# Kernel optimization log

Measured on AMD Instinct MI355X. Metric: run time of the kernel, lower is better.

Reference implementation:

```python
import jax, jax.numpy as jnp
import numpy as np

N = 50000
E = 800000
IN_C = 128
HID = 128
OUT_C = 64
HEADS = 8
HD1 = HID // HEADS   # 16 per-head dim, layer 1 (concat)
HD2 = OUT_C          # 64 per-head dim, layer 2 (concat=False, mean over heads)
NEG_SLOPE = 0.2


def setup_inputs() -> dict:
    key = jax.random.key(0)
    ks = jax.random.split(key, 12)
    x = jax.random.normal(ks[0], (N, IN_C), dtype=jnp.float32)
    edge_index = jax.random.randint(ks[1], (2, E), 0, N, dtype=jnp.int64)
    s1 = 1.0 / np.sqrt(IN_C)
    s2 = 1.0 / np.sqrt(HID)
    W1 = jax.random.normal(ks[2], (IN_C, HEADS * HD1), dtype=jnp.float32) * s1
    att_src1 = jax.random.normal(ks[3], (HEADS, HD1), dtype=jnp.float32) * s1
    att_dst1 = jax.random.normal(ks[4], (HEADS, HD1), dtype=jnp.float32) * s1
    b1 = jnp.zeros((HID,), dtype=jnp.float32)
    W2 = jax.random.normal(ks[5], (HID, HEADS * HD2), dtype=jnp.float32) * s2
    att_src2 = jax.random.normal(ks[6], (HEADS, HD2), dtype=jnp.float32) * s2
    att_dst2 = jax.random.normal(ks[7], (HEADS, HD2), dtype=jnp.float32) * s2
    b2 = jnp.zeros((OUT_C,), dtype=jnp.float32)
    return {"x": x, "edge_index": edge_index,
            "W1": W1, "att_src1": att_src1, "att_dst1": att_dst1, "b1": b1,
            "W2": W2, "att_src2": att_src2, "att_dst2": att_dst2, "b2": b2}


def _gat_conv(x, W, a_src, a_dst, bias, src, dst, heads, head_dim, concat):
    n = x.shape[0]
    h = (x @ W).reshape(n, heads, head_dim)                      # [N,H,D]
    alpha_s = jnp.einsum('nhd,hd->nh', h, a_src)                  # [N,H]
    alpha_d = jnp.einsum('nhd,hd->nh', h, a_dst)                  # [N,H]
    e = jax.nn.leaky_relu(alpha_s[src] + alpha_d[dst], NEG_SLOPE)  # [E,H]
    # segment softmax over edges grouped by destination node
    m = jax.ops.segment_max(e, dst, num_segments=n)               # [N,H]
    m = jnp.where(jnp.isfinite(m), m, 0.0)
    ex = jnp.exp(e - m[dst])
    denom = jax.ops.segment_sum(ex, dst, num_segments=n)
    alpha = ex / (denom[dst] + 1e-16)                             # [E,H]
    out = jax.ops.segment_sum(h[src] * alpha[:, :, None], dst, num_segments=n)  # [N,H,D]
    if concat:
        out = out.reshape(n, heads * head_dim)
    else:
        out = out.mean(axis=1)
    return out + bias


def reference(x, edge_index, W1, att_src1, att_dst1, b1, W2, att_src2, att_dst2, b2):
    # PyG GATConv default add_self_loops=True
    loops = jnp.arange(N, dtype=edge_index.dtype)
    src = jnp.concatenate([edge_index[0], loops])
    dst = jnp.concatenate([edge_index[1], loops])
    h = _gat_conv(x, W1, att_src1, att_dst1, b1, src, dst, HEADS, HD1, True)
    h = jax.nn.relu(h)
    out = _gat_conv(h, W2, att_src2, att_dst2, b2, src, dst, HEADS, HD2, False)
    return out
```

## Files before the change

kernel.cpp:

```cpp
#include <hip/hip_runtime.h>

#define N_NODES 50000
#define N_EDGES 800000
#define ET (N_EDGES + N_NODES)
#define HEADS 8
#define NPAD 50048
#define SCAN_NB 196
#define CAP 96
#define LRS 1032
#define NB_DEG 3321
#define NB_GEMM1 782

typedef __attribute__((ext_vector_type(8))) _Float16 half8;
typedef __attribute__((ext_vector_type(2))) _Float16 half2v;
typedef __attribute__((ext_vector_type(4))) float f32x4;

__device__ __forceinline__ void wave_lds_fence(){
  asm volatile("s_waitcnt lgkmcnt(0)" ::: "memory");
}

__device__ __forceinline__ int edge_src(const int* ei, int e, int is64){
  if (e >= N_EDGES) return e - N_EDGES;
  return is64 ? ei[2*e] : ei[e];
}
__device__ __forceinline__ int edge_dst(const int* ei, int e, int is64){
  if (e >= N_EDGES) return e - N_EDGES;
  return is64 ? ei[2*(N_EDGES + e)] : ei[N_EDGES + e];
}

__global__ void k_init_wprep(const int* __restrict__ ei, int* __restrict__ deg,
                             int* __restrict__ cnt, int* __restrict__ flag,
                             const float* __restrict__ W1, const float* __restrict__ W2,
                             const float* __restrict__ as2, const float* __restrict__ ad2,
                             _Float16* __restrict__ Bp1, _Float16* __restrict__ Bp,
                             float* __restrict__ ws2, float* __restrict__ wd2){
  int b = blockIdx.x;
  int t_ = threadIdx.x;
  if (b < SCAN_NB){
    int i = b*256 + t_;
    if (i < N_NODES){ deg[i] = 0; cnt[i] = 0; }
    if (i == 0){
      int zeros = 0;
      for (int k = 0; k < 64; k++){
        if (ei[2*k + 1] == 0) zeros++;
      }
      *flag = (zeros >= 60) ? 1 : 0;
    }
  } else if (b < SCAN_NB + 256){
    int t = (b - SCAN_NB)*256 + t_;
    int j = t & 7, lane = (t >> 3) & 63, nt = (t >> 9) & 3, kt = t >> 11;
    int k = kt*32 + (lane >> 4)*8 + j;
    int c = nt*16 + (lane & 15);
    int h = k >> 7, kk = k & 127;
    Bp[t] = (_Float16)(0.125f * W2[kk*512 + h*64 + c]);
  } else if (b < SCAN_NB + 320){
    int t = (b - SCAN_NB - 256)*256 + t_;
    int j = t & 7, lane = (t >> 3) & 63, nt = (t >> 9) & 7, kt = t >> 12;
    int k = kt*32 + (lane >> 4)*8 + j;
    int c = nt*16 + (lane & 15);
    Bp1[t] = (_Float16)W1[k*128 + c];
  } else {
    int t = (b - SCAN_NB - 320)*256 + t_;
    int k = t >> 3, h = t & 7;
    float s = 0.f, d = 0.f;
    for (int dd = 0; dd < 64; dd++){
      float w = W2[k*512 + h*64 + dd];
      s += w * as2[h*64 + dd];
      d += w * ad2[h*64 + dd];
    }
    ws2[h*128 + k] = s;
    wd2[h*128 + k] = d;
  }
}

__global__ void __launch_bounds__(256) k_deg_gemm1(
    const int* __restrict__ ei, int* __restrict__ deg, const int* __restrict__ flag,
    const float* __restrict__ x, const _Float16* __restrict__ Bp1,
    _Float16* __restrict__ h1,
    const float* __restrict__ as1, const float* __restrict__ ad1,
    float* __restrict__ als1, float* __restrict__ ald1){
  if (blockIdx.x < NB_DEG){
    int e = blockIdx.x*blockDim.x + threadIdx.x;
    if (e >= ET) return;
    int is64 = *flag;
    int d = edge_dst(ei, e, is64);
    atomicAdd(&deg[d], 1);
    return;
  }
  int bid = blockIdx.x - NB_DEG;
  int tid = threadIdx.x;
  int lane = tid & 63, wv = tid >> 6;
  int n0 = bid*64 + wv*16;
  int rowA = n0 + (lane & 15);
  int koff = (lane >> 4)*8;
  const float* xr = x + (size_t)rowA*128 + koff;
  f32x4 acc[8];
  #pragma unroll
  for (int i = 0; i < 8; i++) acc[i] = (f32x4){0.f,0.f,0.f,0.f};
  bool inb = (rowA < N_NODES);
  #pragma unroll
  for (int kt = 0; kt < 4; kt++){
    half8 af;
    if (inb){
      float4 a0 = *(const float4*)(xr + kt*32);
      float4 a1 = *(const float4*)(xr + kt*32 + 4);
      af = (half8){(_Float16)a0.x,(_Float16)a0.y,(_Float16)a0.z,(_Float16)a0.w,
                   (_Float16)a1.x,(_Float16)a1.y,(_Float16)a1.z,(_Float16)a1.w};
    } else {
      af = (half8){0,0,0,0,0,0,0,0};
    }
    #pragma unroll
    for (int nt = 0; nt < 8; nt++){
      half8 bf = *(const half8*)(Bp1 + (((kt*8 + nt)*64 + lane) << 3));
      acc[nt] = __builtin_amdgcn_mfma_f32_16x16x32_f16(af, bf, acc[nt], 0, 0, 0);
    }
  }
  int m = lane & 15, q = lane >> 4;
  int r0 = n0 + q*4;
  #pragma unroll
  for (int nt = 0; nt < 8; nt++){
    int c = nt*16 + m;
    #pragma unroll
    for (int r = 0; r < 4; r++){
      int n = r0 + r;
      if (n < N_NODES) h1[(size_t)n*128 + c] = (_Float16)acc[nt][r];
    }
  }
  float as1v[8], ad1v[8];
  #pragma unroll
  for (int nt = 0; nt < 8; nt++){
    as1v[nt] = as1[nt*16 + m];
    ad1v[nt] = ad1[nt*16 + m];
  }
  #pragma unroll
  for (int r = 0; r < 4; r++){
    float vs[8], vd[8];
    #pragma unroll
    for (int nt = 0; nt < 8; nt++){
      vs[nt] = acc[nt][r]*as1v[nt];
      vd[nt] = acc[nt][r]*ad1v[nt];
      #pragma unroll
      for (int off = 1; off < 16; off <<= 1){
        vs[nt] += __shfl_xor(vs[nt], off, 64);
        vd[nt] += __shfl_xor(vd[nt], off, 64);
      }
    }
    int n = r0 + r;
    if (m == r && n < N_NODES){
      float4 v0; v0.x = vs[0]; v0.y = vs[1]; v0.z = vs[2]; v0.w = vs[3];
      float4 v1; v1.x = vs[4]; v1.y = vs[5]; v1.z = vs[6]; v1.w = vs[7];
      float4 w0; w0.x = vd[0]; w0.y = vd[1]; w0.z = vd[2]; w0.w = vd[3];
      float4 w1; w1.x = vd[4]; w1.y = vd[5]; w1.z = vd[6]; w1.w = vd[7];
      *(float4*)&als1[n*8]     = v0;
      *(float4*)&als1[n*8 + 4] = v1;
      *(float4*)&ald1[n*8]     = w0;
      *(float4*)&ald1[n*8 + 4] = w1;
    }
  }
}

__global__ void k_scan_part(const int* __restrict__ deg, int* __restrict__ loc,
                            int* __restrict__ part){
  __shared__ int lds[256];
  int t = threadIdx.x, i = blockIdx.x*256 + t;
  int v = (i < N_NODES) ? deg[i] : 0;
  lds[t] = v;
  __syncthreads();
  for (int off = 1; off < 256; off <<= 1){
    int x = (t >= off) ? lds[t - off] : 0;
    __syncthreads();
    lds[t] += x;
    __syncthreads();
  }
  if (i < N_NODES) loc[i] = lds[t] - v;
  if (t == 255) part[blockIdx.x] = lds[255];
}

__global__ void k_scan_carry(int* __restrict__ part, int* __restrict__ carry){
  __shared__ int lds[256];
  int t = threadIdx.x;
  int v = (t < SCAN_NB) ? part[t] : 0;
  lds[t] = v;
  __syncthreads();
  for (int off = 1; off < 256; off <<= 1){
    int x = (t >= off) ? lds[t - off] : 0;
    __syncthreads();
    lds[t] += x;
    __syncthreads();
  }
  if (t < SCAN_NB) carry[t] = lds[t] - v;
}

__global__ void k_scan_add(const int* __restrict__ loc, const int* __restrict__ carry,
                           int* __restrict__ row_ptr){
  int i = blockIdx.x*blockDim.x + threadIdx.x;
  if (i < N_NODES) row_ptr[i] = loc[i] + carry[i >> 8];
  if (i == 0) row_ptr[N_NODES] = ET;
}

__global__ void k_fill(const int* __restrict__ ei, const int* __restrict__ row_ptr,
                       int* __restrict__ cnt, int* __restrict__ col,
                       const int* __restrict__ flag){
  int e = blockIdx.x*blockDim.x + threadIdx.x;
  if (e >= ET) return;
  int is64 = *flag;
  int s = edge_src(ei, e, is64);
  int d = edge_dst(ei, e, is64);
  int pos = atomicAdd(&cnt[d], 1);
  col[row_ptr[d] + pos] = s;
}

__global__ void k_attn_agg1(const _Float16* __restrict__ h1,
    const float* __restrict__ als, const float* __restrict__ ald,
    const int* __restrict__ row_ptr, const int* __restrict__ col,
    const float* __restrict__ bias, _Float16* __restrict__ hr,
    const float* __restrict__ ws2, const float* __restrict__ wd2,
    float* __restrict__ als2, float* __restrict__ ald2){
  __shared__ _Float16 ew_s[4][CAP*8];
  __shared__ int col_s[4][CAP];
  __shared__ _Float16 ot_s[4][136];
  int tid = threadIdx.x;
  int wv = tid >> 6, lane = tid & 63;
  int n = blockIdx.x*4 + wv;
  int beg = row_ptr[n], end = row_ptr[n+1];
  int deg = end - beg;
  int items = deg*8;
  int h = lane & 7;
  float ad = ald[n*8 + h];
  _Float16* es = ew_s[wv];
  int* cs = col_s[wv];
  float l = 0.f;
  int itc = items < CAP*8 ? items : CAP*8;
  int it = lane;
  for (; it < itc; it += 64){
    int e = it >> 3;
    int s = col[beg + e];
    float a = als[s*8 + h] + ad;
    a = (a > 0.f) ? a : 0.2f*a;
    float ex = __expf(a);
    es[it] = (_Float16)ex;
    if ((it & 7) == 0) cs[e] = s;
    l += ex;
  }
  for (; it < items; it += 64){
    int s = col[beg + (it >> 3)];
    float a = als[s*8 + h] + ad;
    a = (a > 0.f) ? a : 0.2f*a;
    l += __expf(a);
  }
  l += __shfl_xor(l, 8, 64);
  l += __shfl_xor(l, 16, 64);
  l += __shfl_xor(l, 32, 64);
  float inv = 1.f / (l + 1e-16f);
  wave_lds_fence();
  int eg = lane >> 4, cb = lane & 15;
  int hq = cb >> 1;
  float invh = __shfl(inv, hq, 64);
  float adh  = __shfl(ad, hq, 64);
  float acc[8];
  #pragma unroll
  for (int k = 0; k < 8; k++) acc[k] = 0.f;
  int degc = deg < CAP ? deg : CAP;
  int j = 0;
  half8 cv;
  if (j + 3 < degc){
    cv = *(const half8*)(h1 + (size_t)cs[j + eg]*128 + cb*8);
  }
  for (; j + 7 < degc; j += 4){
    half8 nv = *(const half8*)(h1 + (size_t)cs[j + 4 + eg]*128 + cb*8);
    float w = (float)es[(j + eg)*8 + hq] * invh;
    #pragma unroll
    for (int k = 0; k < 8; k++) acc[k] += w*(float)cv[k];
    cv = nv;
  }
  if (j + 3 < degc){
    float w = (float)es[(j + eg)*8 + hq] * invh;
    #pragma unroll
    for (int k = 0; k < 8; k++) acc[k] += w*(float)cv[k];
    j += 4;
  }
  if (j < degc){
    int e = j + eg;
    if (e < degc){
      int s = cs[e];
      float w = (float)es[e*8 + hq] * invh;
      half8 v = *(const half8*)(h1 + (size_t)s*128 + cb*8);
      #pragma unroll
      for (int k = 0; k < 8; k++) acc[k] += w*(float)v[k];
    }
  }
  for (int jj = degc; jj < deg; jj += 4){
    int e = jj + eg;
    if (e < deg){
      int s = col[beg + e];
      float a = als[s*8 + hq] + adh;
      a = (a > 0.f) ? a : 0.2f*a;
      float w = __expf(a)*invh;
      half8 v = *(const half8*)(h1 + (size_t)s*128 + cb*8);
      #pragma unroll
      for (int k = 0; k < 8; k++) acc[k] += w*(float)v[k];
    }
  }
  #pragma unroll
  for (int k = 0; k < 8; k++){
    acc[k] += __shfl_xor(acc[k], 16, 64);
    acc[k] += __shfl_xor(acc[k], 32, 64);
  }
  float4 b0 = *(const float4*)(bias + cb*8);
  float4 b1 = *(const float4*)(bias + cb*8 + 4);
  float bb[8] = {b0.x,b0.y,b0.z,b0.w,b1.x,b1.y,b1.z,b1.w};
  half8 oh;
  #pragma unroll
  for (int k = 0; k < 8; k++) oh[k] = (_Float16)fmaxf(acc[k] + bb[k], 0.f);
  if (eg == 0){
    *(half8*)(hr + (size_t)n*128 + cb*8) = oh;
    ((half8*)&ot_s[wv][0])[cb] = oh;
  }
  wave_lds_fence();
  int hh = lane >> 3, seg = lane & 7;
  const half2v* otp = (const half2v*)&ot_s[wv][0];
  const float* wsr = ws2 + hh*128 + seg*16;
  const float* wdr = wd2 + hh*128 + seg*16;
  float vs = 0.f, vd = 0.f;
  #pragma unroll
  for (int i = 0; i < 8; i++){
    half2v v = otp[seg*8 + i];
    float vx = (float)v.x, vy = (float)v.y;
    vs += vx*wsr[2*i] + vy*wsr[2*i + 1];
    vd += vx*wdr[2*i] + vy*wdr[2*i + 1];
  }
  vs += __shfl_xor(vs, 1, 64); vd += __shfl_xor(vd, 1, 64);
  vs += __shfl_xor(vs, 2, 64); vd += __shfl_xor(vd, 2, 64);
  vs += __shfl_xor(vs, 4, 64); vd += __shfl_xor(vd, 4, 64);
  if (seg == 0){
    als2[n*8 + hh] = vs;
    ald2[n*8 + hh] = vd;
  }
}

__global__ void __launch_bounds__(1024) k_attn_agg2(const _Float16* __restrict__ hr,
    const float* __restrict__ als, const float* __restrict__ ald,
    const int* __restrict__ row_ptr, const int* __restrict__ col,
    const _Float16* __restrict__ Bp, const float* __restrict__ b2,
    float* __restrict__ outp){
  __shared__ _Float16 ew_s[16][CAP*8];
  __shared__ int col_s[16][CAP];
  __shared__ _Float16 at[16*LRS];
  int tid = threadIdx.x;
  int wv = tid >> 6, lane = tid & 63;
  int n = blockIdx.x*16 + wv;
  int beg = row_ptr[n], end = row_ptr[n+1];
  int deg = end - beg;
  int items = deg*8;
  int h = lane & 7;
  float ad = ald[n*8 + h];
  _Float16* es = ew_s[wv];
  int* cs = col_s[wv];
  float l = 0.f;
  int itc = items < CAP*8 ? items : CAP*8;
  int it = lane;
  for (; it < itc; it += 64){
    int e = it >> 3;
    int s = col[beg + e];
    float a = als[s*8 + h] + ad;
    a = (a > 0.f) ? a : 0.2f*a;
    float ex = __expf(a);
    es[it] = (_Float16)ex;
    if ((it & 7) == 0) cs[e] = s;
    l += ex;
  }
  for (; it < items; it += 64){
    int s = col[beg + (it >> 3)];
    float a = als[s*8 + h] + ad;
    a = (a > 0.f) ? a : 0.2f*a;
    l += __expf(a);
  }
  l += __shfl_xor(l, 8, 64);
  l += __shfl_xor(l, 16, 64);
  l += __shfl_xor(l, 32, 64);
  float inv = 1.f / (l + 1e-16f);
  wave_lds_fence();
  int hp = lane >> 4, cb = lane & 15;
  float invA = __shfl(inv, 2*hp, 64);
  float invB = __shfl(inv, 2*hp + 1, 64);
  half2v inv2; inv2.x = (_Float16)invA; inv2.y = (_Float16)invB;
  half2v acc_a[4], acc_b[4];
  #pragma unroll
  for (int i = 0; i < 4; i++){
    acc_a[i] = (half2v){(_Float16)0.f, (_Float16)0.f};
    acc_b[i] = (half2v){(_Float16)0.f, (_Float16)0.f};
  }
  int degc = deg < CAP ? deg : CAP;
  const _Float16* esw = es + 2*hp;
  int j = 0;
  half8 cv0, cv1, cv2, cv3;
  if (j + 3 < degc){
    cv0 = *(const half8*)(hr + (size_t)cs[j+0]*128 + cb*8);
    cv1 = *(const half8*)(hr + (size_t)cs[j+1]*128 + cb*8);
    cv2 = *(const half8*)(hr + (size_t)cs[j+2]*128 + cb*8);
    cv3 = *(const half8*)(hr + (size_t)cs[j+3]*128 + cb*8);
  }
  for (; j + 7 < degc; j += 4){
    half8 nv0 = *(const half8*)(hr + (size_t)cs[j+4]*128 + cb*8);
    half8 nv1 = *(const half8*)(hr + (size_t)cs[j+5]*128 + cb*8);
    half8 nv2 = *(const half8*)(hr + (size_t)cs[j+6]*128 + cb*8);
    half8 nv3 = *(const half8*)(hr + (size_t)cs[j+7]*128 + cb*8);
    half2v w0 = *(const half2v*)(esw + (j+0)*8) * inv2;
    half2v w1 = *(const half2v*)(esw + (j+1)*8) * inv2;
    half2v w2 = *(const half2v*)(esw + (j+2)*8) * inv2;
    half2v w3 = *(const half2v*)(esw + (j+3)*8) * inv2;
    #pragma unroll
    for (int k = 0; k < 4; k++){
      half2v t;
      t = (half2v){cv0[2*k], cv0[2*k+1]};
      acc_a[k] += (half2v){w0.x, w0.x} * t;
      acc_b[k] += (half2v){w0.y, w0.y} * t;
      t = (half2v){cv1[2*k], cv1[2*k+1]};
      acc_a[k] += (half2v){w1.x, w1.x} * t;
      acc_b[k] += (half2v){w1.y, w1.y} * t;
      t = (half2v){cv2[2*k], cv2[2*k+1]};
      acc_a[k] += (half2v){w2.x, w2.x} * t;
      acc_b[k] += (half2v){w2.y, w2.y} * t;
      t = (half2v){cv3[2*k], cv3[2*k+1]};
      acc_a[k] += (half2v){w3.x, w3.x} * t;
      acc_b[k] += (half2v){w3.y, w3.y} * t;
    }
    cv0 = nv0; cv1 = nv1; cv2 = nv2; cv3 = nv3;
  }
  if (j + 3 < degc){
    half2v w0 = *(const half2v*)(esw + (j+0)*8) * inv2;
    half2v w1 = *(const half2v*)(esw + (j+1)*8) * inv2;
    half2v w2 = *(const half2v*)(esw + (j+2)*8) * inv2;
    half2v w3 = *(const half2v*)(esw + (j+3)*8) * inv2;
    #pragma unroll
    for (int k = 0; k < 4; k++){
      half2v t;
      t = (half2v){cv0[2*k], cv0[2*k+1]};
      acc_a[k] += (half2v){w0.x, w0.x} * t;
      acc_b[k] += (half2v){w0.y, w0.y} * t;
      t = (half2v){cv1[2*k], cv1[2*k+1]};
      acc_a[k] += (half2v){w1.x, w1.x} * t;
      acc_b[k] += (half2v){w1.y, w1.y} * t;
      t = (half2v){cv2[2*k], cv2[2*k+1]};
      acc_a[k] += (half2v){w2.x, w2.x} * t;
      acc_b[k] += (half2v){w2.y, w2.y} * t;
      t = (half2v){cv3[2*k], cv3[2*k+1]};
      acc_a[k] += (half2v){w3.x, w3.x} * t;
      acc_b[k] += (half2v){w3.y, w3.y} * t;
    }
    j += 4;
  }
  for (; j < degc; j++){
    int s = cs[j];
    half2v w = *(const half2v*)(esw + j*8) * inv2;
    half8 v = *(const half8*)(hr + (size_t)s*128 + cb*8);
    #pragma unroll
    for (int k = 0; k < 4; k++){
      half2v t = (half2v){v[2*k], v[2*k+1]};
      acc_a[k] += (half2v){w.x, w.x} * t;
      acc_b[k] += (half2v){w.y, w.y} * t;
    }
  }
  if (deg > CAP){
    float2 adv = *(const float2*)(ald + (size_t)n*8 + 2*hp);
    for (; j < deg; j++){
      int s = col[beg + j];
      float2 alv = *(const float2*)(als + (size_t)s*8 + 2*hp);
      float a0 = alv.x + adv.x; a0 = (a0 > 0.f) ? a0 : 0.2f*a0;
      float a1 = alv.y + adv.y; a1 = (a1 > 0.f) ? a1 : 0.2f*a1;
      _Float16 w0 = (_Float16)(__expf(a0)*invA);
      _Float16 w1 = (_Float16)(__expf(a1)*invB);
      half8 v = *(const half8*)(hr + (size_t)s*128 + cb*8);
      #pragma unroll
      for (int k = 0; k < 4; k++){
        half2v t = (half2v){v[2*k], v[2*k+1]};
        acc_a[k] += (half2v){w0, w0} * t;
        acc_b[k] += (half2v){w1, w1} * t;
      }
    }
  }
  _Float16* ar = at + wv*LRS + (2*hp)*128 + cb*8;
  half8 oa, ob;
  #pragma unroll
  for (int k = 0; k < 4; k++){
    oa[2*k] = acc_a[k].x; oa[2*k+1] = acc_a[k].y;
    ob[2*k] = acc_b[k].x; ob[2*k+1] = acc_b[k].y;
  }
  *(half8*)ar = oa;
  *(half8*)(ar + 128) = ob;
  __syncthreads();
  if (wv >= 4) return;
  int m = lane & 15, q = lane >> 4;
  const _Float16* arow = at + m*LRS + q*8;
  f32x4 cacc = (f32x4){0.f,0.f,0.f,0.f};
  #pragma unroll 4
  for (int kt = 0; kt < 32; kt++){
    half8 af = *(const half8*)(arow + kt*32);
    half8 bf = *(const half8*)(Bp + (((kt*4 + wv)*64 + lane) << 3));
    cacc = __builtin_amdgcn_mfma_f32_16x16x32_f16(af, bf, cacc, 0, 0, 0);
  }
  int c = wv*16 + m;
  float bb = b2[c];
  #pragma unroll
  for (int r = 0; r < 4; r++){
    int nrow = blockIdx.x*16 + q*4 + r;
    outp[(size_t)nrow*64 + c] = cacc[r] + bb;
  }
}

extern "C" void kernel_launch(void* const* d_in, const int* in_sizes, int n_in,
                              void* d_out, int out_size, void* d_ws, size_t ws_size,
                              hipStream_t stream){
  const float* x   = (const float*)d_in[0];
  const int*   ei  = (const int*)d_in[1];
  const float* W1  = (const float*)d_in[2];
  const float* as1 = (const float*)d_in[3];
  const float* ad1 = (const float*)d_in[4];
  const float* b1  = (const float*)d_in[5];
  const float* W2  = (const float*)d_in[6];
  const float* as2 = (const float*)d_in[7];
  const float* ad2 = (const float*)d_in[8];
  const float* b2  = (const float*)d_in[9];
  float* outp = (float*)d_out;

  char* p = (char*)d_ws;
  auto alloc = [&](size_t bytes) -> void* {
    void* r = (void*)p;
    p += (bytes + 255) & ~(size_t)255;
    return r;
  };
  _Float16* h1  = (_Float16*)alloc((size_t)NPAD*128*2);
  _Float16* hr  = (_Float16*)alloc((size_t)N_NODES*128*2);
  float* als1 = (float*)alloc((size_t)N_NODES*8*4);
  float* ald1 = (float*)alloc((size_t)N_NODES*8*4);
  float* als2 = (float*)alloc((size_t)N_NODES*8*4);
  float* ald2 = (float*)alloc((size_t)N_NODES*8*4);
  int* row_ptr = (int*)alloc((size_t)(N_NODES+1)*4);
  int* deg  = (int*)alloc((size_t)N_NODES*4);
  int* cnt  = (int*)alloc((size_t)N_NODES*4);
  int* col  = (int*)alloc((size_t)ET*4);
  int* loc  = (int*)alloc((size_t)N_NODES*4);
  int* part = (int*)alloc(256*4);
  int* carry= (int*)alloc(256*4);
  int* flag = (int*)alloc(256);
  float* ws2 = (float*)alloc(1024*4);
  float* wd2 = (float*)alloc(1024*4);
  _Float16* Bp1 = (_Float16*)alloc((size_t)16384*2);
  _Float16* Bp  = (_Float16*)alloc((size_t)65536*2);

  dim3 b256(256);
  k_init_wprep<<<SCAN_NB + 324, b256, 0, stream>>>(ei, deg, cnt, flag,
                                                   W1, W2, as2, ad2,
                                                   Bp1, Bp, ws2, wd2);
  k_deg_gemm1<<<NB_DEG + NB_GEMM1, b256, 0, stream>>>(ei, deg, flag,
                                                      x, Bp1, h1, as1, ad1,
                                                      als1, ald1);
  k_scan_part<<<SCAN_NB, b256, 0, stream>>>(deg, loc, part);
  k_scan_carry<<<1, b256, 0, stream>>>(part, carry);
  k_scan_add<<<SCAN_NB, b256, 0, stream>>>(loc, carry, row_ptr);
  k_fill<<<(ET+255)/256, b256, 0, stream>>>(ei, row_ptr, cnt, col, flag);
  k_attn_agg1<<<N_NODES/4, b256, 0, stream>>>(h1, als1, ald1, row_ptr, col,
                                              b1, hr, ws2, wd2, als2, ald2);
  k_attn_agg2<<<N_NODES/16, dim3(1024), 0, stream>>>(hr, als2, ald2, row_ptr, col,
                                                     Bp, b2, outp);
}
```

Measured before the change: 323.5 us.

## Precompute layer-1 edge attention weights during CSR fill

The CSR fill kernel now also computes the unnormalised layer-1 attention weights (leaky-relu then exp of src+dst logits) for each edge and stores them as fp16 in CSR order. The aggregation kernel then reads these contiguous weights instead of gathering per-source logits and recomputing exp. The software-prefetch double buffering of h1 rows in the main aggregation loop is also removed for a simpler loop. This adds an extra 13.6 MB write plus read of edge weights and extra random gathers in k_fill.

```diff
diff --git a/kernel.cpp b/kernel.cpp
--- a/kernel.cpp
+++ b/kernel.cpp
@@ -200,18 +200,35 @@
 
 __global__ void k_fill(const int* __restrict__ ei, const int* __restrict__ row_ptr,
                        int* __restrict__ cnt, int* __restrict__ col,
-                       const int* __restrict__ flag){
+                       const int* __restrict__ flag,
+                       const float* __restrict__ als1, const float* __restrict__ ald1,
+                       _Float16* __restrict__ ew1){
   int e = blockIdx.x*blockDim.x + threadIdx.x;
   if (e >= ET) return;
   int is64 = *flag;
   int s = edge_src(ei, e, is64);
   int d = edge_dst(ei, e, is64);
   int pos = atomicAdd(&cnt[d], 1);
-  col[row_ptr[d] + pos] = s;
+  int slot = row_ptr[d] + pos;
+  col[slot] = s;
+  float4 a0 = *(const float4*)(als1 + (size_t)s*8);
+  float4 a1 = *(const float4*)(als1 + (size_t)s*8 + 4);
+  float4 d0 = *(const float4*)(ald1 + (size_t)d*8);
+  float4 d1 = *(const float4*)(ald1 + (size_t)d*8 + 4);
+  float av[8] = {a0.x+d0.x, a0.y+d0.y, a0.z+d0.z, a0.w+d0.w,
+                 a1.x+d1.x, a1.y+d1.y, a1.z+d1.z, a1.w+d1.w};
+  half8 w;
+  #pragma unroll
+  for (int h = 0; h < 8; h++){
+    float a = av[h];
+    a = (a > 0.f) ? a : 0.2f*a;
+    w[h] = (_Float16)__expf(a);
+  }
+  *(half8*)(ew1 + (size_t)slot*8) = w;
 }
 
 __global__ void k_attn_agg1(const _Float16* __restrict__ h1,
-    const float* __restrict__ als, const float* __restrict__ ald,
+    const _Float16* __restrict__ ew1,
     const int* __restrict__ row_ptr, const int* __restrict__ col,
     const float* __restrict__ bias, _Float16* __restrict__ hr,
     const float* __restrict__ ws2, const float* __restrict__ wd2,
@@ -225,28 +242,20 @@
   int beg = row_ptr[n], end = row_ptr[n+1];
   int deg = end - beg;
   int items = deg*8;
-  int h = lane & 7;
-  float ad = ald[n*8 + h];
   _Float16* es = ew_s[wv];
   int* cs = col_s[wv];
+  const _Float16* ewr = ew1 + (size_t)beg*8;
   float l = 0.f;
   int itc = items < CAP*8 ? items : CAP*8;
   int it = lane;
   for (; it < itc; it += 64){
-    int e = it >> 3;
-    int s = col[beg + e];
-    float a = als[s*8 + h] + ad;
-    a = (a > 0.f) ? a : 0.2f*a;
-    float ex = __expf(a);
-    es[it] = (_Float16)ex;
-    if ((it & 7) == 0) cs[e] = s;
-    l += ex;
+    _Float16 w = ewr[it];
+    es[it] = w;
+    l += (float)w;
+    if ((it & 7) == 0) cs[it >> 3] = col[beg + (it >> 3)];
   }
   for (; it < items; it += 64){
-    int s = col[beg + (it >> 3)];
-    float a = als[s*8 + h] + ad;
-    a = (a > 0.f) ? a : 0.2f*a;
-    l += __expf(a);
+    l += (float)ewr[it];
   }
   l += __shfl_xor(l, 8, 64);
   l += __shfl_xor(l, 16, 64);
@@ -256,28 +265,18 @@
   int eg = lane >> 4, cb = lane & 15;
   int hq = cb >> 1;
   float invh = __shfl(inv, hq, 64);
-  float adh  = __shfl(ad, hq, 64);
   float acc[8];
   #pragma unroll
   for (int k = 0; k < 8; k++) acc[k] = 0.f;
   int degc = deg < CAP ? deg : CAP;
   int j = 0;
-  half8 cv;
-  if (j + 3 < degc){
-    cv = *(const half8*)(h1 + (size_t)cs[j + eg]*128 + cb*8);
-  }
-  for (; j + 7 < degc; j += 4){
-    half8 nv = *(const half8*)(h1 + (size_t)cs[j + 4 + eg]*128 + cb*8);
-    float w = (float)es[(j + eg)*8 + hq] * invh;
-    #pragma unroll
-    for (int k = 0; k < 8; k++) acc[k] += w*(float)cv[k];
-    cv = nv;
-  }
-  if (j + 3 < degc){
-    float w = (float)es[(j + eg)*8 + hq] * invh;
-    #pragma unroll
-    for (int k = 0; k < 8; k++) acc[k] += w*(float)cv[k];
-    j += 4;
+  for (; j + 3 < degc; j += 4){
+    int e = j + eg;
+    int s = cs[e];
+    float w = (float)es[e*8 + hq] * invh;
+    half8 v = *(const half8*)(h1 + (size_t)s*128 + cb*8);
+    #pragma unroll
+    for (int k = 0; k < 8; k++) acc[k] += w*(float)v[k];
   }
   if (j < degc){
     int e = j + eg;
@@ -293,9 +292,7 @@
     int e = jj + eg;
     if (e < deg){
       int s = col[beg + e];
-      float a = als[s*8 + hq] + adh;
-      a = (a > 0.f) ? a : 0.2f*a;
-      float w = __expf(a)*invh;
+      float w = (float)ewr[e*8 + hq] * invh;
       half8 v = *(const half8*)(h1 + (size_t)s*128 + cb*8);
       #pragma unroll
       for (int k = 0; k < 8; k++) acc[k] += w*(float)v[k];
@@ -531,6 +528,7 @@
   };
   _Float16* h1  = (_Float16*)alloc((size_t)NPAD*128*2);
   _Float16* hr  = (_Float16*)alloc((size_t)N_NODES*128*2);
+  _Float16* ew1 = (_Float16*)alloc((size_t)ET*8*2);
   float* als1 = (float*)alloc((size_t)N_NODES*8*4);
   float* ald1 = (float*)alloc((size_t)N_NODES*8*4);
   float* als2 = (float*)alloc((size_t)N_NODES*8*4);
@@ -558,8 +556,9 @@
   k_scan_part<<<SCAN_NB, b256, 0, stream>>>(deg, loc, part);
   k_scan_carry<<<1, b256, 0, stream>>>(part, carry);
   k_scan_add<<<SCAN_NB, b256, 0, stream>>>(loc, carry, row_ptr);
-  k_fill<<<(ET+255)/256, b256, 0, stream>>>(ei, row_ptr, cnt, col, flag);
-  k_attn_agg1<<<N_NODES/4, b256, 0, stream>>>(h1, als1, ald1, row_ptr, col,
+  k_fill<<<(ET+255)/256, b256, 0, stream>>>(ei, row_ptr, cnt, col, flag,
+                                            als1, ald1, ew1);
+  k_attn_agg1<<<N_NODES/4, b256, 0, stream>>>(h1, ew1, row_ptr, col,
                                               b1, hr, ws2, wd2, als2, ald2);
   k_attn_agg2<<<N_NODES/16, dim3(1024), 0, stream>>>(hr, als2, ald2, row_ptr, col,
                                                      Bp, b2, outp);
```

New measurement: 322.3 us. No clear change (-0.4%).
